# Performance work log

Hardware: AMD Instinct MI355X
Metric: run time of the kernel (lower is better)

The kernel has to match this reference:

```python
import jax, jax.numpy as jnp
import numpy as np

B, L, DX, DQ = 8, 4096, 128, 128


def setup_inputs() -> dict:
    key = jax.random.key(0)
    ks = jax.random.split(key, 16)
    g = lambda k, shp, fan: jax.random.normal(k, shp, jnp.float32) * (1.0 / np.sqrt(fan))
    return {
        'x': jax.random.normal(ks[0], (B, L, DX), jnp.float32),
        'c': jax.random.normal(ks[1], (B, DQ), jnp.float32),
        # CrossAttention('add') params (all Linear weights stored as (in, out))
        'W1': g(ks[2], (DX, DX), DX),          # w1, bias frozen at 0
        'W2': g(ks[3], (DQ, DX), DQ),          # w2, bias frozen at 0
        'wt_w': g(ks[4], (DX,), DX),           # wt: dx -> 1, bias frozen at 0
        'bsa': jnp.zeros((DX,), jnp.float32),
        # csa pairwise-score params
        'Wsa1': g(ks[5], (DX, DX), DX),        # bias frozen at 0
        'Wsa2': g(ks[6], (DX, DX), DX),        # bias frozen at 0
        'wsat_w': g(ks[7], (DX,), DX),         # wsat: dx -> 1
        'wsat_b': jnp.zeros((), jnp.float32),
        'bsa1': jnp.zeros((DX,), jnp.float32),
        # PositionwiseFeedForward(dx, dx)
        'pfn_w1': g(ks[8], (DX, DX), DX),
        'pfn_b1': jnp.zeros((DX,), jnp.float32),
        'pfn_w2': g(ks[9], (DX, DX), DX),
        'pfn_b2': jnp.zeros((DX,), jnp.float32),
        'ln_g': jnp.ones((DX,), jnp.float32),
        'ln_b': jnp.zeros((DX,), jnp.float32),
    }


def reference(x, c, W1, W2, wt_w, bsa, Wsa1, Wsa2, wsat_w, wsat_b, bsa1,
              pfn_w1, pfn_b1, pfn_w2, pfn_b2, ln_g, ln_b):
    seq_len = x.shape[-2]
    # ---- CrossAttention, mode='add': p = softmax(wt(w1(x) + w2(c) + bsa), dim=-2) ----
    wx = jnp.einsum('bld,de->ble', x, W1)                 # (B, L, dx)
    wq = jnp.einsum('bd,de->be', c, W2)                   # (B, dx)
    logits = jnp.einsum('ble,e->bl', wx + wq[:, None, :] + bsa, wt_w)
    p = jax.nn.softmax(logits, axis=-1)[..., None]        # softmax over L -> (B, L, 1)
    h = x * p                                             # (B, L, dx)
    # ---- pairwise additive scores: wsat(Wsa1(h)_i + Wsa2(h)_j + bsa1) ----
    # wsat is linear, so the (B,L,L,dx) tensor decomposes exactly into rank-1 terms.
    si = jnp.einsum('ble,e->bl', jnp.einsum('bld,de->ble', h, Wsa1), wsat_w)  # (B, L)
    sj = jnp.einsum('ble,e->bl', jnp.einsum('bld,de->ble', h, Wsa2), wsat_w)  # (B, L)
    const = jnp.dot(bsa1, wsat_w) + wsat_b
    scores = jax.nn.sigmoid(si[:, :, None] + sj[:, None, :] + const)          # (B, L, L)
    # mask diagonal with -inf then softmax over last dim (j)
    diag = jnp.eye(seq_len, dtype=bool)
    scores = jnp.where(diag, -jnp.inf, scores)
    A = jax.nn.softmax(scores, axis=-1)                   # (B, L, L)
    # ui = sum_i A[b,i,j] * x[b,j,:]  (faithful to fcsa * x.unsqueeze(1) summed over dim 1)
    ui = x * jnp.sum(A, axis=1)[..., None]                # (B, L, dx)
    # ---- PositionwiseFeedForward with residual + LayerNorm(eps=1e-6); dropout=eval/identity ----
    y = jnp.maximum(jnp.einsum('bld,de->ble', ui, pfn_w1) + pfn_b1, 0.0)
    y = jnp.einsum('ble,ed->bld', y, pfn_w2) + pfn_b2 + ui
    mu = jnp.mean(y, axis=-1, keepdims=True)
    var = jnp.mean(jnp.square(y - mu), axis=-1, keepdims=True)
    return (y - mu) / jnp.sqrt(var + 1e-6) * ln_g + ln_b
```

## Files before the change

kernel.cpp:

```cpp
#include <hip/hip_runtime.h>


#define SEQ 4096
#define NB 8
#define DXC 128
#define SQRTE 1.6487212707001282f

__device__ __forceinline__ float wave_sum(float v) {
#pragma unroll
  for (int m = 32; m >= 1; m >>= 1) v += __shfl_xor(v, m);
  return v;
}

__device__ __forceinline__ void get_ck(float* ck) {
  ck[0] = 1.0f;
  ck[1] = 0.25f;
  ck[2] = 0.03125f;
  ck[3] = -7.0f / 384.0f;
  ck[4] = -31.0f / 6144.0f;
  ck[5] = 177.0f / 122880.0f;
  ck[6] = 2017.0f / 2949120.0f;
}

__device__ __forceinline__ float binomf(int k, int m) {
  const float B[7][7] = {
      {1, 0, 0, 0, 0, 0, 0},  {1, 1, 0, 0, 0, 0, 0},   {1, 2, 1, 0, 0, 0, 0},
      {1, 3, 3, 1, 0, 0, 0},  {1, 4, 6, 4, 1, 0, 0},   {1, 5, 10, 10, 5, 1, 0},
      {1, 6, 15, 20, 15, 6, 1}};
  return B[k][m];
}

__device__ __forceinline__ float g_exact(float t) {
  float sg = 1.0f / (1.0f + __expf(-t));
  return __expf(sg);
}

__global__ __launch_bounds__(256) void prep_vecs(
    const float* __restrict__ W1, const float* __restrict__ W2,
    const float* __restrict__ Wsa1, const float* __restrict__ Wsa2,
    const float* __restrict__ wt_w, const float* __restrict__ wsat_w,
    float* __restrict__ vecs) {
  int wave = (blockIdx.x * 256 + threadIdx.x) >> 6;
  int lane = threadIdx.x & 63;
  int m = wave >> 7, d = wave & 127;
  const float* W = (m == 0) ? W1 : (m == 1) ? W2 : (m == 2) ? Wsa1 : Wsa2;
  const float* v = (m < 2) ? wt_w : wsat_w;
  float2 a = ((const float2*)(W + d * DXC))[lane];
  float2 b = ((const float2*)v)[lane];
  float s = wave_sum(a.x * b.x + a.y * b.y);
  if (lane == 0) vecs[m * DXC + d] = s;
}

__global__ __launch_bounds__(256) void rowdots(
    const float* __restrict__ x, const float* __restrict__ vecs,
    float* __restrict__ t0, float* __restrict__ t1, float* __restrict__ t2) {
  int row = (blockIdx.x * 256 + threadIdx.x) >> 6;
  int lane = threadIdx.x & 63;
  float2 xv = ((const float2*)(x + (size_t)row * DXC))[lane];
  float2 a = ((const float2*)(vecs + 0))[lane];
  float2 b = ((const float2*)(vecs + 256))[lane];
  float2 d = ((const float2*)(vecs + 384))[lane];
  float s0 = wave_sum(xv.x * a.x + xv.y * a.y);
  float s1 = wave_sum(xv.x * b.x + xv.y * b.y);
  float s2 = wave_sum(xv.x * d.x + xv.y * d.y);
  if (lane == 0) { t0[row] = s0; t1[row] = s1; t2[row] = s2; }
}

__global__ __launch_bounds__(1024) void softmax_sisj(
    const float* __restrict__ t0, const float* __restrict__ t1,
    const float* __restrict__ t2, const float* __restrict__ c,
    const float* __restrict__ bsa, const float* __restrict__ wt_w,
    const float* __restrict__ bsa1, const float* __restrict__ wsat_w,
    const float* __restrict__ wsat_b, const float* __restrict__ v2,
    float* __restrict__ si, float* __restrict__ sj, float* __restrict__ Pout) {
  __shared__ float red[16];
  __shared__ float red6[16][6];
  __shared__ float bc[4];
  __shared__ float Sv[8];
  int b = blockIdx.x, tid = threadIdx.x;
  if (tid < 64) {
    float2 cv = ((const float2*)(c + b * DXC))[tid];
    float2 vv = ((const float2*)v2)[tid];
    float2 ba = ((const float2*)bsa)[tid];
    float2 wt = ((const float2*)wt_w)[tid];
    float s = wave_sum(cv.x * vv.x + cv.y * vv.y + ba.x * wt.x + ba.y * wt.y);
    float2 b1 = ((const float2*)bsa1)[tid];
    float2 ww = ((const float2*)wsat_w)[tid];
    float t = wave_sum(b1.x * ww.x + b1.y * ww.y);
    if (tid == 0) { bc[2] = s; bc[3] = t + wsat_b[0]; }
  }
  float4 l4 = ((const float4*)(t0 + b * SEQ))[tid];
  __syncthreads();
  float cbv = bc[2], ccst = bc[3];
  l4.x += cbv; l4.y += cbv; l4.z += cbv; l4.w += cbv;
  float m = fmaxf(fmaxf(l4.x, l4.y), fmaxf(l4.z, l4.w));
#pragma unroll
  for (int s = 32; s >= 1; s >>= 1) m = fmaxf(m, __shfl_xor(m, s));
  if ((tid & 63) == 0) red[tid >> 6] = m;
  __syncthreads();
  if (tid < 16) {
    float v = red[tid];
#pragma unroll
    for (int s = 8; s >= 1; s >>= 1) v = fmaxf(v, __shfl_xor(v, s));
    if (tid == 0) bc[0] = v;
  }
  __syncthreads();
  float M = bc[0];
  float e0 = __expf(l4.x - M), e1 = __expf(l4.y - M);
  float e2 = __expf(l4.z - M), e3 = __expf(l4.w - M);
  float s = (e0 + e1) + (e2 + e3);
#pragma unroll
  for (int sh = 32; sh >= 1; sh >>= 1) s += __shfl_xor(s, sh);
  if ((tid & 63) == 0) red[tid >> 6] = s;
  __syncthreads();
  if (tid < 16) {
    float v = red[tid];
#pragma unroll
    for (int sh = 8; sh >= 1; sh >>= 1) v += __shfl_xor(v, sh);
    if (tid == 0) bc[1] = v;
  }
  __syncthreads();
  float inv = 1.0f / bc[1];
  float4 a = ((const float4*)(t1 + b * SEQ))[tid];
  float4 bb = ((const float4*)(t2 + b * SEQ))[tid];
  float4 so, sjo;
  so.x = e0 * inv * a.x + ccst;  so.y = e1 * inv * a.y + ccst;
  so.z = e2 * inv * a.z + ccst;  so.w = e3 * inv * a.w + ccst;
  sjo.x = e0 * inv * bb.x; sjo.y = e1 * inv * bb.y;
  sjo.z = e2 * inv * bb.z; sjo.w = e3 * inv * bb.w;
  ((float4*)(si + b * SEQ))[tid] = so;
  ((float4*)(sj + b * SEQ))[tid] = sjo;
  float sm[6] = {0.f, 0.f, 0.f, 0.f, 0.f, 0.f};
  float vals[4] = {sjo.x, sjo.y, sjo.z, sjo.w};
#pragma unroll
  for (int e = 0; e < 4; ++e) {
    float t = vals[e];
#pragma unroll
    for (int n = 0; n < 6; ++n) { sm[n] += t; t *= vals[e]; }
  }
#pragma unroll
  for (int n = 0; n < 6; ++n) sm[n] = wave_sum(sm[n]);
  if ((tid & 63) == 0) {
#pragma unroll
    for (int n = 0; n < 6; ++n) red6[tid >> 6][n] = sm[n];
  }
  __syncthreads();
  if (tid < 6) {
    float acc = 0.f;
#pragma unroll
    for (int w = 0; w < 16; ++w) acc += red6[w][tid];
    Sv[tid + 1] = acc;
  }
  if (tid == 6) Sv[0] = (float)SEQ;
  __syncthreads();
  if (tid < 7) {
    float ck[7];
    get_ck(ck);
    float acc = 0.f;
    for (int n = 0; n <= 6 - tid; ++n)
      acc += ck[tid + n] * binomf(tid + n, tid) * Sv[n];
    Pout[b * 8 + tid] = SQRTE * acc;
  }
}

__global__ __launch_bounds__(1024) void zq(
    const float* __restrict__ si, const float* __restrict__ sj,
    const float* __restrict__ P, float* __restrict__ dcol,
    float* __restrict__ Qout) {
  __shared__ float red7[16][7];
  __shared__ float Tv[8];
  int b = blockIdx.x, tid = threadIdx.x;
  float Pl[7];
#pragma unroll
  for (int n = 0; n < 7; ++n) Pl[n] = P[b * 8 + n];
  float acc[7] = {0.f, 0.f, 0.f, 0.f, 0.f, 0.f, 0.f};
#pragma unroll
  for (int r = 0; r < 4; ++r) {
    int i = b * SEQ + r * 1024 + tid;
    float a = si[i];
    float bb = sj[i];
    float zf = ((((((Pl[6] * a + Pl[5]) * a + Pl[4]) * a + Pl[3]) * a + Pl[2]) * a
                + Pl[1]) * a) + Pl[0];
    float d = g_exact(a + bb);
    float iz = 1.0f / (zf - d);
    dcol[i] = d * iz;
    float p = iz;
    acc[0] += p;
#pragma unroll
    for (int n = 1; n < 7; ++n) { p *= a; acc[n] += p; }
  }
#pragma unroll
  for (int n = 0; n < 7; ++n) acc[n] = wave_sum(acc[n]);
  if ((tid & 63) == 0) {
#pragma unroll
    for (int n = 0; n < 7; ++n) red7[tid >> 6][n] = acc[n];
  }
  __syncthreads();
  if (tid < 7) {
    float t = 0.f;
#pragma unroll
    for (int w = 0; w < 16; ++w) t += red7[w][tid];
    Tv[tid] = t;
  }
  __syncthreads();
  if (tid < 7) {
    float ck[7];
    get_ck(ck);
    float acc2 = 0.f;
    for (int n = 0; n <= 6 - tid; ++n)
      acc2 += ck[tid + n] * binomf(tid + n, tid) * Tv[n];
    Qout[b * 8 + tid] = SQRTE * acc2;
  }
}

__global__ __launch_bounds__(256) void ffn_ln(
    const float* __restrict__ x, const float* __restrict__ sj,
    const float* __restrict__ dcol, const float* __restrict__ Q,
    const float* __restrict__ W1p, const float* __restrict__ b1,
    const float* __restrict__ W2p, const float* __restrict__ b2,
    const float* __restrict__ lng, const float* __restrict__ lnb,
    float* __restrict__ out) {
  __shared__ __align__(16) float ts[64 * 132];
  __shared__ float cs[64];
  int tid = threadIdx.x;
  int base = blockIdx.x * 64;
  int b = blockIdx.x >> 6;
  if (tid < 64) {
    int row = base + tid;
    float bb = sj[row];
    float q0 = Q[b * 8 + 0], q1 = Q[b * 8 + 1], q2 = Q[b * 8 + 2];
    float q3 = Q[b * 8 + 3], q4 = Q[b * 8 + 4], q5 = Q[b * 8 + 5];
    float q6 = Q[b * 8 + 6];
    cs[tid] = ((((((q6 * bb + q5) * bb + q4) * bb + q3) * bb + q2) * bb + q1) * bb
              + q0) - dcol[row];
  }
  __syncthreads();
  for (int k = tid; k < 64 * DXC; k += 256) {
    int r = k >> 7, d = k & 127;
    ts[r * 132 + d] = x[(size_t)(base + r) * DXC + d] * cs[r];
  }
  __syncthreads();
  int cg = tid & 31, r0 = tid >> 5;
  const float* tsrow = &ts[r0 * 8 * 132];
  float acc[8][4];
#pragma unroll
  for (int k = 0; k < 8; ++k) acc[k][0] = acc[k][1] = acc[k][2] = acc[k][3] = 0.f;
  for (int d = 0; d < DXC; ++d) {
    float4 w = *(const float4*)&W1p[d * DXC + cg * 4];
#pragma unroll
    for (int k = 0; k < 8; ++k) {
      float u = tsrow[k * 132 + d];
      acc[k][0] = fmaf(u, w.x, acc[k][0]);
      acc[k][1] = fmaf(u, w.y, acc[k][1]);
      acc[k][2] = fmaf(u, w.z, acc[k][2]);
      acc[k][3] = fmaf(u, w.w, acc[k][3]);
    }
  }
  float4 b1v = *(const float4*)&b1[cg * 4];
  __syncthreads();
#pragma unroll
  for (int k = 0; k < 8; ++k) {
    float4 y;
    y.x = fmaxf(acc[k][0] + b1v.x, 0.f);
    y.y = fmaxf(acc[k][1] + b1v.y, 0.f);
    y.z = fmaxf(acc[k][2] + b1v.z, 0.f);
    y.w = fmaxf(acc[k][3] + b1v.w, 0.f);
    *(float4*)&ts[(r0 * 8 + k) * 132 + cg * 4] = y;
  }
  __syncthreads();
#pragma unroll
  for (int k = 0; k < 8; ++k) acc[k][0] = acc[k][1] = acc[k][2] = acc[k][3] = 0.f;
  for (int e = 0; e < DXC; ++e) {
    float4 w = *(const float4*)&W2p[e * DXC + cg * 4];
#pragma unroll
    for (int k = 0; k < 8; ++k) {
      float yv = tsrow[k * 132 + e];
      acc[k][0] = fmaf(yv, w.x, acc[k][0]);
      acc[k][1] = fmaf(yv, w.y, acc[k][1]);
      acc[k][2] = fmaf(yv, w.z, acc[k][2]);
      acc[k][3] = fmaf(yv, w.w, acc[k][3]);
    }
  }
  float4 b2v = *(const float4*)&b2[cg * 4];
  float4 gv = *(const float4*)&lng[cg * 4];
  float4 bev = *(const float4*)&lnb[cg * 4];
#pragma unroll
  for (int k = 0; k < 8; ++k) {
    int row = base + r0 * 8 + k;
    float csr = cs[r0 * 8 + k];
    float4 xr = *(const float4*)&x[(size_t)row * DXC + cg * 4];
    float z0 = acc[k][0] + b2v.x + xr.x * csr;
    float z1 = acc[k][1] + b2v.y + xr.y * csr;
    float z2 = acc[k][2] + b2v.z + xr.z * csr;
    float z3 = acc[k][3] + b2v.w + xr.w * csr;
    float s = (z0 + z1) + (z2 + z3);
    float sq = (z0 * z0 + z1 * z1) + (z2 * z2 + z3 * z3);
#pragma unroll
    for (int m = 16; m >= 1; m >>= 1) {
      s += __shfl_xor(s, m);
      sq += __shfl_xor(sq, m);
    }
    float mu = s * 0.0078125f;
    float var = sq * 0.0078125f - mu * mu;
    float rstd = 1.0f / sqrtf(var + 1e-6f);
    float4 o;
    o.x = (z0 - mu) * rstd * gv.x + bev.x;
    o.y = (z1 - mu) * rstd * gv.y + bev.y;
    o.z = (z2 - mu) * rstd * gv.z + bev.z;
    o.w = (z3 - mu) * rstd * gv.w + bev.w;
    *(float4*)&out[(size_t)row * DXC + cg * 4] = o;
  }
}

extern "C" void kernel_launch(void* const* d_in, const int* in_sizes, int n_in,
                              void* d_out, int out_size, void* d_ws, size_t ws_size,
                              hipStream_t stream) {
  const float* x = (const float*)d_in[0];
  const float* cc = (const float*)d_in[1];
  const float* W1 = (const float*)d_in[2];
  const float* W2 = (const float*)d_in[3];
  const float* wt_w = (const float*)d_in[4];
  const float* bsa = (const float*)d_in[5];
  const float* Wsa1 = (const float*)d_in[6];
  const float* Wsa2 = (const float*)d_in[7];
  const float* wsat_w = (const float*)d_in[8];
  const float* wsat_b = (const float*)d_in[9];
  const float* bsa1 = (const float*)d_in[10];
  const float* pw1 = (const float*)d_in[11];
  const float* pb1 = (const float*)d_in[12];
  const float* pw2 = (const float*)d_in[13];
  const float* pb2 = (const float*)d_in[14];
  const float* lng = (const float*)d_in[15];
  const float* lnb = (const float*)d_in[16];
  float* out = (float*)d_out;
  float* ws = (float*)d_ws;

  const int NR = NB * SEQ;
  float* vecs = ws;
  float* P = ws + 512;
  float* Q = ws + 576;
  float* t0 = ws + 1024;
  float* t1 = t0 + NR;
  float* t2 = t1 + NR;
  float* si = t2 + NR;
  float* sj = si + NR;
  float* dcol = sj + NR;

  prep_vecs<<<128, 256, 0, stream>>>(W1, W2, Wsa1, Wsa2, wt_w, wsat_w, vecs);
  rowdots<<<NR / 4, 256, 0, stream>>>(x, vecs, t0, t1, t2);
  softmax_sisj<<<NB, 1024, 0, stream>>>(t0, t1, t2, cc, bsa, wt_w, bsa1, wsat_w,
                                        wsat_b, vecs + 128, si, sj, P);
  zq<<<NB, 1024, 0, stream>>>(si, sj, P, dcol, Q);
  ffn_ln<<<NR / 64, 256, 0, stream>>>(x, sj, dcol, Q, pw1, pb1, pw2, pb2, lng,
                                      lnb, out);
}
```

Baseline: 151.5 us.

## Use bf16 MFMA for FFN, fuse softmax with zq, pack transposed weights

```diff
diff --git a/kernel.cpp b/kernel.cpp
--- a/kernel.cpp
+++ b/kernel.cpp
@@ -5,11 +5,21 @@
 #define NB 8
 #define DXC 128
 #define SQRTE 1.6487212707001282f
+#define Y1S 136
+
+typedef __attribute__((ext_vector_type(8))) short short8;
+typedef __attribute__((ext_vector_type(4))) float f32x4;
 
 __device__ __forceinline__ float wave_sum(float v) {
 #pragma unroll
   for (int m = 32; m >= 1; m >>= 1) v += __shfl_xor(v, m);
   return v;
+}
+
+__device__ __forceinline__ unsigned short f2bf(float f) {
+  unsigned int u = __float_as_uint(f);
+  unsigned int r = (u + 0x7FFFu + ((u >> 16) & 1u)) >> 16;
+  return (unsigned short)r;
 }
 
 __device__ __forceinline__ void get_ck(float* ck) {
@@ -35,20 +45,33 @@
   return __expf(sg);
 }
 
-__global__ __launch_bounds__(256) void prep_vecs(
+__global__ __launch_bounds__(256) void prep_pack(
     const float* __restrict__ W1, const float* __restrict__ W2,
     const float* __restrict__ Wsa1, const float* __restrict__ Wsa2,
     const float* __restrict__ wt_w, const float* __restrict__ wsat_w,
-    float* __restrict__ vecs) {
-  int wave = (blockIdx.x * 256 + threadIdx.x) >> 6;
-  int lane = threadIdx.x & 63;
-  int m = wave >> 7, d = wave & 127;
-  const float* W = (m == 0) ? W1 : (m == 1) ? W2 : (m == 2) ? Wsa1 : Wsa2;
-  const float* v = (m < 2) ? wt_w : wsat_w;
-  float2 a = ((const float2*)(W + d * DXC))[lane];
-  float2 b = ((const float2*)v)[lane];
-  float s = wave_sum(a.x * b.x + a.y * b.y);
-  if (lane == 0) vecs[m * DXC + d] = s;
+    const float* __restrict__ pw1, const float* __restrict__ pw2,
+    float* __restrict__ vecs, unsigned short* __restrict__ Wt1,
+    unsigned short* __restrict__ Wt2) {
+  if (blockIdx.x < 128) {
+    int wave = (blockIdx.x * 256 + threadIdx.x) >> 6;
+    int lane = threadIdx.x & 63;
+    int m = wave >> 7, d = wave & 127;
+    const float* W = (m == 0) ? W1 : (m == 1) ? W2 : (m == 2) ? Wsa1 : Wsa2;
+    const float* v = (m < 2) ? wt_w : wsat_w;
+    float2 a = ((const float2*)(W + d * DXC))[lane];
+    float2 b = ((const float2*)v)[lane];
+    float s = wave_sum(a.x * b.x + a.y * b.y);
+    if (lane == 0) vecs[m * DXC + d] = s;
+  } else {
+    int id = (blockIdx.x - 128) * 256 + threadIdx.x;
+    int which = id >> 14;
+    int k = id & 16383;
+    int eo = k >> 7, d = k & 127;
+    if (which == 0)
+      Wt1[eo * DXC + d] = f2bf(pw1[d * DXC + eo]);
+    else
+      Wt2[eo * DXC + d] = f2bf(pw2[d * DXC + eo]);
+  }
 }
 
 __global__ __launch_bounds__(256) void rowdots(
@@ -66,17 +89,19 @@
   if (lane == 0) { t0[row] = s0; t1[row] = s1; t2[row] = s2; }
 }
 
-__global__ __launch_bounds__(1024) void softmax_sisj(
+__global__ __launch_bounds__(1024) void softmax_zq(
     const float* __restrict__ t0, const float* __restrict__ t1,
     const float* __restrict__ t2, const float* __restrict__ c,
     const float* __restrict__ bsa, const float* __restrict__ wt_w,
     const float* __restrict__ bsa1, const float* __restrict__ wsat_w,
     const float* __restrict__ wsat_b, const float* __restrict__ v2,
-    float* __restrict__ si, float* __restrict__ sj, float* __restrict__ Pout) {
+    float* __restrict__ sj, float* __restrict__ dcol,
+    float* __restrict__ Qout) {
   __shared__ float red[16];
-  __shared__ float red6[16][6];
+  __shared__ float red7[16][7];
   __shared__ float bc[4];
   __shared__ float Sv[8];
+  __shared__ float Ps[7];
   int b = blockIdx.x, tid = threadIdx.x;
   if (tid < 64) {
     float2 cv = ((const float2*)(c + b * DXC))[tid];
@@ -121,34 +146,34 @@
   }
   __syncthreads();
   float inv = 1.0f / bc[1];
-  float4 a = ((const float4*)(t1 + b * SEQ))[tid];
-  float4 bb = ((const float4*)(t2 + b * SEQ))[tid];
-  float4 so, sjo;
-  so.x = e0 * inv * a.x + ccst;  so.y = e1 * inv * a.y + ccst;
-  so.z = e2 * inv * a.z + ccst;  so.w = e3 * inv * a.w + ccst;
-  sjo.x = e0 * inv * bb.x; sjo.y = e1 * inv * bb.y;
-  sjo.z = e2 * inv * bb.z; sjo.w = e3 * inv * bb.w;
-  ((float4*)(si + b * SEQ))[tid] = so;
-  ((float4*)(sj + b * SEQ))[tid] = sjo;
-  float sm[6] = {0.f, 0.f, 0.f, 0.f, 0.f, 0.f};
-  float vals[4] = {sjo.x, sjo.y, sjo.z, sjo.w};
-#pragma unroll
-  for (int e = 0; e < 4; ++e) {
-    float t = vals[e];
-#pragma unroll
-    for (int n = 0; n < 6; ++n) { sm[n] += t; t *= vals[e]; }
-  }
-#pragma unroll
-  for (int n = 0; n < 6; ++n) sm[n] = wave_sum(sm[n]);
-  if ((tid & 63) == 0) {
-#pragma unroll
-    for (int n = 0; n < 6; ++n) red6[tid >> 6][n] = sm[n];
+  float4 a4 = ((const float4*)(t1 + b * SEQ))[tid];
+  float4 bb4 = ((const float4*)(t2 + b * SEQ))[tid];
+  float av[4], bv[4];
+  av[0] = e0 * inv * a4.x + ccst; av[1] = e1 * inv * a4.y + ccst;
+  av[2] = e2 * inv * a4.z + ccst; av[3] = e3 * inv * a4.w + ccst;
+  bv[0] = e0 * inv * bb4.x; bv[1] = e1 * inv * bb4.y;
+  bv[2] = e2 * inv * bb4.z; bv[3] = e3 * inv * bb4.w;
+  ((float4*)(sj + b * SEQ))[tid] = make_float4(bv[0], bv[1], bv[2], bv[3]);
+  {
+    float sm[6] = {0.f, 0.f, 0.f, 0.f, 0.f, 0.f};
+#pragma unroll
+    for (int e = 0; e < 4; ++e) {
+      float t = bv[e];
+#pragma unroll
+      for (int n = 0; n < 6; ++n) { sm[n] += t; t *= bv[e]; }
+    }
+#pragma unroll
+    for (int n = 0; n < 6; ++n) sm[n] = wave_sum(sm[n]);
+    if ((tid & 63) == 0) {
+#pragma unroll
+      for (int n = 0; n < 6; ++n) red7[tid >> 6][n] = sm[n];
+    }
   }
   __syncthreads();
   if (tid < 6) {
     float acc = 0.f;
 #pragma unroll
-    for (int w = 0; w < 16; ++w) acc += red6[w][tid];
+    for (int w = 0; w < 16; ++w) acc += red7[w][tid];
     Sv[tid + 1] = acc;
   }
   if (tid == 6) Sv[0] = (float)SEQ;
@@ -159,36 +184,28 @@
     float acc = 0.f;
     for (int n = 0; n <= 6 - tid; ++n)
       acc += ck[tid + n] * binomf(tid + n, tid) * Sv[n];
-    Pout[b * 8 + tid] = SQRTE * acc;
-  }
-}
-
-__global__ __launch_bounds__(1024) void zq(
-    const float* __restrict__ si, const float* __restrict__ sj,
-    const float* __restrict__ P, float* __restrict__ dcol,
-    float* __restrict__ Qout) {
-  __shared__ float red7[16][7];
-  __shared__ float Tv[8];
-  int b = blockIdx.x, tid = threadIdx.x;
-  float Pl[7];
-#pragma unroll
-  for (int n = 0; n < 7; ++n) Pl[n] = P[b * 8 + n];
+    Ps[tid] = SQRTE * acc;
+  }
+  __syncthreads();
+  float P0 = Ps[0], P1 = Ps[1], P2 = Ps[2], P3 = Ps[3], P4 = Ps[4],
+        P5 = Ps[5], P6 = Ps[6];
   float acc[7] = {0.f, 0.f, 0.f, 0.f, 0.f, 0.f, 0.f};
-#pragma unroll
-  for (int r = 0; r < 4; ++r) {
-    int i = b * SEQ + r * 1024 + tid;
-    float a = si[i];
-    float bb = sj[i];
-    float zf = ((((((Pl[6] * a + Pl[5]) * a + Pl[4]) * a + Pl[3]) * a + Pl[2]) * a
-                + Pl[1]) * a) + Pl[0];
-    float d = g_exact(a + bb);
+  float4 dc;
+  float* dcp = (float*)&dc;
+#pragma unroll
+  for (int e = 0; e < 4; ++e) {
+    float a = av[e];
+    float zf = ((((((P6 * a + P5) * a + P4) * a + P3) * a + P2) * a + P1) * a)
+               + P0;
+    float d = g_exact(a + bv[e]);
     float iz = 1.0f / (zf - d);
-    dcol[i] = d * iz;
+    dcp[e] = d * iz;
     float p = iz;
     acc[0] += p;
 #pragma unroll
     for (int n = 1; n < 7; ++n) { p *= a; acc[n] += p; }
   }
+  ((float4*)(dcol + b * SEQ))[tid] = dc;
 #pragma unroll
   for (int n = 0; n < 7; ++n) acc[n] = wave_sum(acc[n]);
   if ((tid & 63) == 0) {
@@ -200,7 +217,7 @@
     float t = 0.f;
 #pragma unroll
     for (int w = 0; w < 16; ++w) t += red7[w][tid];
-    Tv[tid] = t;
+    red[tid] = t;
   }
   __syncthreads();
   if (tid < 7) {
@@ -208,20 +225,21 @@
     get_ck(ck);
     float acc2 = 0.f;
     for (int n = 0; n <= 6 - tid; ++n)
-      acc2 += ck[tid + n] * binomf(tid + n, tid) * Tv[n];
+      acc2 += ck[tid + n] * binomf(tid + n, tid) * red[n];
     Qout[b * 8 + tid] = SQRTE * acc2;
   }
 }
 
-__global__ __launch_bounds__(256) void ffn_ln(
+__global__ __launch_bounds__(256) void ffn_mfma(
     const float* __restrict__ x, const float* __restrict__ sj,
     const float* __restrict__ dcol, const float* __restrict__ Q,
-    const float* __restrict__ W1p, const float* __restrict__ b1,
-    const float* __restrict__ W2p, const float* __restrict__ b2,
+    const unsigned short* __restrict__ Wt1,
+    const unsigned short* __restrict__ Wt2,
+    const float* __restrict__ b1, const float* __restrict__ b2,
     const float* __restrict__ lng, const float* __restrict__ lnb,
     float* __restrict__ out) {
-  __shared__ __align__(16) float ts[64 * 132];
   __shared__ float cs[64];
+  __shared__ __align__(16) unsigned short y1[64 * Y1S];
   int tid = threadIdx.x;
   int base = blockIdx.x * 64;
   int b = blockIdx.x >> 6;
@@ -231,84 +249,96 @@
     float q0 = Q[b * 8 + 0], q1 = Q[b * 8 + 1], q2 = Q[b * 8 + 2];
     float q3 = Q[b * 8 + 3], q4 = Q[b * 8 + 4], q5 = Q[b * 8 + 5];
     float q6 = Q[b * 8 + 6];
-    cs[tid] = ((((((q6 * bb + q5) * bb + q4) * bb + q3) * bb + q2) * bb + q1) * bb
-              + q0) - dcol[row];
-  }
-  __syncthreads();
-  for (int k = tid; k < 64 * DXC; k += 256) {
-    int r = k >> 7, d = k & 127;
-    ts[r * 132 + d] = x[(size_t)(base + r) * DXC + d] * cs[r];
-  }
-  __syncthreads();
-  int cg = tid & 31, r0 = tid >> 5;
-  const float* tsrow = &ts[r0 * 8 * 132];
-  float acc[8][4];
-#pragma unroll
-  for (int k = 0; k < 8; ++k) acc[k][0] = acc[k][1] = acc[k][2] = acc[k][3] = 0.f;
-  for (int d = 0; d < DXC; ++d) {
-    float4 w = *(const float4*)&W1p[d * DXC + cg * 4];
-#pragma unroll
-    for (int k = 0; k < 8; ++k) {
-      float u = tsrow[k * 132 + d];
-      acc[k][0] = fmaf(u, w.x, acc[k][0]);
-      acc[k][1] = fmaf(u, w.y, acc[k][1]);
-      acc[k][2] = fmaf(u, w.z, acc[k][2]);
-      acc[k][3] = fmaf(u, w.w, acc[k][3]);
-    }
-  }
-  float4 b1v = *(const float4*)&b1[cg * 4];
-  __syncthreads();
-#pragma unroll
-  for (int k = 0; k < 8; ++k) {
-    float4 y;
-    y.x = fmaxf(acc[k][0] + b1v.x, 0.f);
-    y.y = fmaxf(acc[k][1] + b1v.y, 0.f);
-    y.z = fmaxf(acc[k][2] + b1v.z, 0.f);
-    y.w = fmaxf(acc[k][3] + b1v.w, 0.f);
-    *(float4*)&ts[(r0 * 8 + k) * 132 + cg * 4] = y;
-  }
-  __syncthreads();
-#pragma unroll
-  for (int k = 0; k < 8; ++k) acc[k][0] = acc[k][1] = acc[k][2] = acc[k][3] = 0.f;
-  for (int e = 0; e < DXC; ++e) {
-    float4 w = *(const float4*)&W2p[e * DXC + cg * 4];
-#pragma unroll
-    for (int k = 0; k < 8; ++k) {
-      float yv = tsrow[k * 132 + e];
-      acc[k][0] = fmaf(yv, w.x, acc[k][0]);
-      acc[k][1] = fmaf(yv, w.y, acc[k][1]);
-      acc[k][2] = fmaf(yv, w.z, acc[k][2]);
-      acc[k][3] = fmaf(yv, w.w, acc[k][3]);
-    }
-  }
-  float4 b2v = *(const float4*)&b2[cg * 4];
-  float4 gv = *(const float4*)&lng[cg * 4];
-  float4 bev = *(const float4*)&lnb[cg * 4];
-#pragma unroll
-  for (int k = 0; k < 8; ++k) {
-    int row = base + r0 * 8 + k;
-    float csr = cs[r0 * 8 + k];
-    float4 xr = *(const float4*)&x[(size_t)row * DXC + cg * 4];
-    float z0 = acc[k][0] + b2v.x + xr.x * csr;
-    float z1 = acc[k][1] + b2v.y + xr.y * csr;
-    float z2 = acc[k][2] + b2v.z + xr.z * csr;
-    float z3 = acc[k][3] + b2v.w + xr.w * csr;
-    float s = (z0 + z1) + (z2 + z3);
-    float sq = (z0 * z0 + z1 * z1) + (z2 * z2 + z3 * z3);
-#pragma unroll
-    for (int m = 16; m >= 1; m >>= 1) {
-      s += __shfl_xor(s, m);
-      sq += __shfl_xor(sq, m);
+    cs[tid] = ((((((q6 * bb + q5) * bb + q4) * bb + q3) * bb + q2) * bb + q1)
+              * bb + q0) - dcol[row];
+  }
+  __syncthreads();
+  int lane = tid & 63, wave = tid >> 6;
+  int n16 = lane & 15, quad = lane >> 4;
+  int m0 = wave * 16;
+  int rowA = base + m0 + n16;
+  float csA = cs[m0 + n16];
+  const float4* xr = (const float4*)(x + (size_t)rowA * DXC);
+  short8 afr[4];
+#pragma unroll
+  for (int cc = 0; cc < 4; ++cc) {
+    float4 p0 = xr[cc * 8 + quad * 2];
+    float4 p1 = xr[cc * 8 + quad * 2 + 1];
+    short8 af;
+    af[0] = (short)f2bf(p0.x * csA); af[1] = (short)f2bf(p0.y * csA);
+    af[2] = (short)f2bf(p0.z * csA); af[3] = (short)f2bf(p0.w * csA);
+    af[4] = (short)f2bf(p1.x * csA); af[5] = (short)f2bf(p1.y * csA);
+    af[6] = (short)f2bf(p1.z * csA); af[7] = (short)f2bf(p1.w * csA);
+    afr[cc] = af;
+  }
+#pragma unroll
+  for (int nt = 0; nt < 8; ++nt) {
+    const unsigned short* wrow = Wt1 + (nt * 16 + n16) * DXC;
+    f32x4 a = {0.f, 0.f, 0.f, 0.f};
+#pragma unroll
+    for (int cc = 0; cc < 4; ++cc) {
+      short8 bf = *(const short8*)(wrow + cc * 32 + quad * 8);
+      a = __builtin_amdgcn_mfma_f32_16x16x32_bf16(afr[cc], bf, a, 0, 0, 0);
+    }
+    float b1v = b1[nt * 16 + n16];
+#pragma unroll
+    for (int r = 0; r < 4; ++r) {
+      float yv = fmaxf(a[r] + b1v, 0.f);
+      y1[(m0 + quad * 4 + r) * Y1S + nt * 16 + n16] = f2bf(yv);
+    }
+  }
+  __syncthreads();
+  const unsigned short* yrow = &y1[(m0 + n16) * Y1S];
+  short8 afr2[4];
+#pragma unroll
+  for (int cc = 0; cc < 4; ++cc)
+    afr2[cc] = *(const short8*)(yrow + cc * 32 + quad * 8);
+  f32x4 acc2[8];
+#pragma unroll
+  for (int nt = 0; nt < 8; ++nt) {
+    const unsigned short* wrow = Wt2 + (nt * 16 + n16) * DXC;
+    f32x4 a = {0.f, 0.f, 0.f, 0.f};
+#pragma unroll
+    for (int cc = 0; cc < 4; ++cc) {
+      short8 bf = *(const short8*)(wrow + cc * 32 + quad * 8);
+      a = __builtin_amdgcn_mfma_f32_16x16x32_bf16(afr2[cc], bf, a, 0, 0, 0);
+    }
+    acc2[nt] = a;
+  }
+  float b2v[8], lgv[8], lbv[8];
+#pragma unroll
+  for (int nt = 0; nt < 8; ++nt) {
+    int col = nt * 16 + n16;
+    b2v[nt] = b2[col]; lgv[nt] = lng[col]; lbv[nt] = lnb[col];
+  }
+#pragma unroll
+  for (int r = 0; r < 4; ++r) {
+    int rl = m0 + quad * 4 + r;
+    int row = base + rl;
+    float csr = cs[rl];
+    const float* xrow = x + (size_t)row * DXC;
+    float z[8];
+    float s = 0.f, sq = 0.f;
+#pragma unroll
+    for (int nt = 0; nt < 8; ++nt) {
+      int col = nt * 16 + n16;
+      float zz = acc2[nt][r] + b2v[nt] + xrow[col] * csr;
+      z[nt] = zz; s += zz; sq += zz * zz;
+    }
+#pragma unroll
+    for (int mm = 8; mm >= 1; mm >>= 1) {
+      s += __shfl_xor(s, mm);
+      sq += __shfl_xor(sq, mm);
     }
     float mu = s * 0.0078125f;
     float var = sq * 0.0078125f - mu * mu;
     float rstd = 1.0f / sqrtf(var + 1e-6f);
-    float4 o;
-    o.x = (z0 - mu) * rstd * gv.x + bev.x;
-    o.y = (z1 - mu) * rstd * gv.y + bev.y;
-    o.z = (z2 - mu) * rstd * gv.z + bev.z;
-    o.w = (z3 - mu) * rstd * gv.w + bev.w;
-    *(float4*)&out[(size_t)row * DXC + cg * 4] = o;
+    float* orow = out + (size_t)row * DXC;
+#pragma unroll
+    for (int nt = 0; nt < 8; ++nt) {
+      int col = nt * 16 + n16;
+      orow[col] = (z[nt] - mu) * rstd * lgv[nt] + lbv[nt];
+    }
   }
 }
 
@@ -337,20 +367,20 @@
 
   const int NR = NB * SEQ;
   float* vecs = ws;
-  float* P = ws + 512;
-  float* Q = ws + 576;
+  float* Q = ws + 512;
   float* t0 = ws + 1024;
   float* t1 = t0 + NR;
   float* t2 = t1 + NR;
-  float* si = t2 + NR;
-  float* sj = si + NR;
+  float* sj = t2 + NR;
   float* dcol = sj + NR;
-
-  prep_vecs<<<128, 256, 0, stream>>>(W1, W2, Wsa1, Wsa2, wt_w, wsat_w, vecs);
+  unsigned short* Wt1 = (unsigned short*)(ws + 164864);
+  unsigned short* Wt2 = (unsigned short*)(ws + 164864 + 8192);
+
+  prep_pack<<<256, 256, 0, stream>>>(W1, W2, Wsa1, Wsa2, wt_w, wsat_w, pw1,
+                                     pw2, vecs, Wt1, Wt2);
   rowdots<<<NR / 4, 256, 0, stream>>>(x, vecs, t0, t1, t2);
-  softmax_sisj<<<NB, 1024, 0, stream>>>(t0, t1, t2, cc, bsa, wt_w, bsa1, wsat_w,
-                                        wsat_b, vecs + 128, si, sj, P);
-  zq<<<NB, 1024, 0, stream>>>(si, sj, P, dcol, Q);
-  ffn_ln<<<NR / 64, 256, 0, stream>>>(x, sj, dcol, Q, pw1, pb1, pw2, pb2, lng,
-                                      lnb, out);
-}
+  softmax_zq<<<NB, 1024, 0, stream>>>(t0, t1, t2, cc, bsa, wt_w, bsa1, wsat_w,
+                                      wsat_b, vecs + 128, sj, dcol, Q);
+  ffn_mfma<<<NR / 64, 256, 0, stream>>>(x, sj, dcol, Q, Wt1, Wt2, pb1, pb2,
+                                        lng, lnb, out);
+}
```

After: 137.4 us. 9.4% less time.
